# Optimization experiments

Measured on AMD Instinct MI355X. Metric: run time of the kernel, lower is better.

The kernel has to match this reference:

```python
import jax, jax.numpy as jnp
import numpy as np

B, V, F, H, W = 2, 8000, 1500, 128, 128
EPS_AREA = 1e-8
EPS_Z = 1e-4


def setup_inputs() -> dict:
    key = jax.random.key(0)
    k1, k2, k3 = jax.random.split(key, 3)
    verts = jax.random.normal(k1, (B, V, 3), jnp.float32) * 0.5
    faces = jax.random.randint(k2, (F, 3), 0, V)
    R = jnp.tile(jnp.eye(3, dtype=jnp.float32)[None], (B, 1, 1)) + 0.01 * jax.random.normal(k3, (B, 3, 3), jnp.float32)
    T = jnp.tile(jnp.array([0.0, 0.0, 3.0], jnp.float32)[None], (B, 1))
    focal = jnp.float32(2.0)
    return {"verts": verts, "R": R, "T": T, "focal": focal, "faces": faces}


def _edge(ax, ay, bx, by, px, py):
    return (px - ax) * (by - ay) - (py - ay) * (bx - ax)


def _project(verts, R, T, focal):
    # world -> view -> screen (NDC xy); screen z replaced by view z (as in MeshRasterizer.transform)
    vv = jnp.einsum('bvi,bij->bvj', verts, R) + T[:, None, :]   # [B,V,3]
    z = vv[..., 2:3]
    xy = focal * vv[..., :2] / z
    return jnp.concatenate([xy, z], axis=-1)                     # [B,V,3]


def _rasterize(vs, faces):
    fv = vs[:, faces]                                            # [B,F,3,3] (vert, xyz)
    # PyTorch3D NDC pixel centers: +X left, +Y up
    xg = 1.0 - 2.0 * (jnp.arange(W, dtype=jnp.float32) + 0.5) / W
    yg = 1.0 - 2.0 * (jnp.arange(H, dtype=jnp.float32) + 0.5) / H
    pyy, pxx = jnp.meshgrid(yg, xg, indexing='ij')
    pxf, pyf = pxx.reshape(-1), pyy.reshape(-1)                  # [P]

    fx = fv[..., 0][:, None]                                     # [B,1,F,3]
    fy = fv[..., 1][:, None]
    fz = fv[..., 2][:, None]
    px = pxf[None, :, None]                                      # [1,P,1]
    py = pyf[None, :, None]

    area = _edge(fv[..., 0, 0], fv[..., 0, 1], fv[..., 1, 0], fv[..., 1, 1],
                 fv[..., 2, 0], fv[..., 2, 1])[:, None]          # [B,1,F]
    area_safe = jnp.where(jnp.abs(area) > EPS_AREA, area, EPS_AREA)

    w0 = _edge(fx[..., 1], fy[..., 1], fx[..., 2], fy[..., 2], px, py)
    w1 = _edge(fx[..., 2], fy[..., 2], fx[..., 0], fy[..., 0], px, py)
    w2 = _edge(fx[..., 0], fy[..., 0], fx[..., 1], fy[..., 1], px, py)
    b0, b1, b2 = w0 / area_safe, w1 / area_safe, w2 / area_safe  # [B,P,F]

    inside = (b0 >= 0) & (b1 >= 0) & (b2 >= 0) & (jnp.abs(area) > EPS_AREA)
    zp = b0 * fz[..., 0] + b1 * fz[..., 1] + b2 * fz[..., 2]     # [B,P,F]
    valid = inside & (zp > EPS_Z)

    zmask = jnp.where(valid, zp, jnp.inf)
    idx = jnp.argmin(zmask, axis=-1)                             # [B,P]
    zmin = jnp.min(zmask, axis=-1)
    hit = jnp.isfinite(zmin)                                     # [B,P]

    # gather winning face per pixel, recompute bary / z / dists only for it
    bfv = fv[jnp.arange(B)[:, None], idx]                        # [B,P,3,3]
    bx, by, bz = bfv[..., 0], bfv[..., 1], bfv[..., 2]           # [B,P,3]
    pxp, pyp = pxf[None, :], pyf[None, :]

    a2 = _edge(bx[..., 0], by[..., 0], bx[..., 1], by[..., 1], bx[..., 2], by[..., 2])
    a2s = jnp.where(jnp.abs(a2) > EPS_AREA, a2, EPS_AREA)
    c0 = _edge(bx[..., 1], by[..., 1], bx[..., 2], by[..., 2], pxp, pyp) / a2s
    c1 = _edge(bx[..., 2], by[..., 2], bx[..., 0], by[..., 0], pxp, pyp) / a2s
    c2 = _edge(bx[..., 0], by[..., 0], bx[..., 1], by[..., 1], pxp, pyp) / a2s
    bary = jnp.stack([c0, c1, c2], axis=-1)                      # [B,P,3]
    zbest = jnp.sum(bary * bz, axis=-1)                          # [B,P]

    def seg_d2(ax, ay, bx_, by_):
        dx, dy = bx_ - ax, by_ - ay
        l2 = jnp.maximum(dx * dx + dy * dy, 1e-12)
        t = jnp.clip(((pxp - ax) * dx + (pyp - ay) * dy) / l2, 0.0, 1.0)
        ex, ey = ax + t * dx - pxp, ay + t * dy - pyp
        return ex * ex + ey * ey

    d2 = jnp.minimum(jnp.minimum(
        seg_d2(bx[..., 0], by[..., 0], bx[..., 1], by[..., 1]),
        seg_d2(bx[..., 1], by[..., 1], bx[..., 2], by[..., 2])),
        seg_d2(bx[..., 2], by[..., 2], bx[..., 0], by[..., 0]))
    inside_b = (c0 >= 0) & (c1 >= 0) & (c2 >= 0)
    dists = jnp.where(inside_b, -d2, d2)                         # signed sq. distance

    neg1 = jnp.float32(-1.0)
    pix_to_face = jnp.where(hit, idx, -1).astype(jnp.int32).reshape(B, H, W, 1)
    zbuf = jnp.where(hit, zbest, neg1).reshape(B, H, W, 1)
    bary_o = jnp.where(hit[..., None], bary, neg1).reshape(B, H, W, 1, 3)
    dists_o = jnp.where(hit, dists, neg1).reshape(B, H, W, 1)
    return pix_to_face, zbuf, bary_o, dists_o


def reference(verts, R, T, focal, faces):
    vs = _project(verts, R, T, focal)
    return _rasterize(vs, faces)
```

## Files before the change

kernel.cpp:

```cpp
#include <hip/hip_runtime.h>
#include <math.h>

#pragma clang fp contract(off)

#define Bn 2
#define Vn 8000
#define Fn 1500
#define Hn 128
#define Wn 128
#define EPS_AREA_F 1e-8f
#define EPS_Z_F 1e-4f
#define NWORD 24
#define NSEG 8
#define NSLICE 8
#define TPB (NSEG * 64)
#define MAXL 1536


__global__ void zero_kernel(unsigned long long* __restrict__ bins,
                            unsigned long long* __restrict__ keybuf) {
    int i = blockIdx.x * blockDim.x + threadIdx.x;
    int n1 = Bn * 256 * NWORD;
    int n2 = Bn * Hn * Wn;
    if (i < n1) bins[i] = 0ull;
    else if (i < n1 + n2) keybuf[i - n1] = ~0ull;
}

__global__ void proj_kernel(const float* __restrict__ verts, const float* __restrict__ R,
                            const float* __restrict__ T, const float* __restrict__ focal,
                            const int* __restrict__ faces,
                            float4* __restrict__ recS, unsigned* __restrict__ bboxT) {
    int t = blockIdx.x * blockDim.x + threadIdx.x;
    if (t >= Bn * Fn) return;
    int b = t / Fn;
    int f = t - b * Fn;
    const float* Rb = R + b * 9;
    const float* Tb = T + b * 3;
    float fo = focal[0];
    float X[3], Y[3], Z[3];
    for (int k = 0; k < 3; ++k) {
        int vi = faces[f * 3 + k];
        const float* v = verts + ((size_t)b * Vn + vi) * 3;
        float v0 = v[0], v1 = v[1], v2 = v[2];
        float vx = v0 * Rb[0] + v1 * Rb[3] + v2 * Rb[6] + Tb[0];
        float vy = v0 * Rb[1] + v1 * Rb[4] + v2 * Rb[7] + Tb[1];
        float vz = v0 * Rb[2] + v1 * Rb[5] + v2 * Rb[8] + Tb[2];
        X[k] = (fo * vx) / vz;
        Y[k] = (fo * vy) / vz;
        Z[k] = vz;
    }
    float area = (X[2] - X[0]) * (Y[1] - Y[0]) - (Y[2] - Y[0]) * (X[1] - X[0]);
    float as = (fabsf(area) > EPS_AREA_F) ? area : EPS_AREA_F;
    recS[t * 3 + 0] = make_float4(X[0], Y[0], X[1], Y[1]);
    recS[t * 3 + 1] = make_float4(X[2], Y[2], area, as);
    recS[t * 3 + 2] = make_float4(Z[0], Z[1], Z[2], 0.0f);

    unsigned pk = 0xFFFFFFFFu;
    if (fabsf(area) > EPS_AREA_F) {
        float xmin = fminf(X[0], fminf(X[1], X[2]));
        float xmax = fmaxf(X[0], fmaxf(X[1], X[2]));
        float ymin = fminf(Y[0], fminf(Y[1], Y[2]));
        float ymax = fmaxf(Y[0], fmaxf(Y[1], Y[2]));
        const float D = 0.02f;
        float wlo = ceilf(64.0f * (1.0f - xmax - D) - 0.5f);
        float whi = floorf(64.0f * (1.0f - xmin + D) - 0.5f);
        float hlo = ceilf(64.0f * (1.0f - ymax - D) - 0.5f);
        float hhi = floorf(64.0f * (1.0f - ymin + D) - 0.5f);
        wlo = fmaxf(wlo, 0.0f); whi = fminf(whi, 127.0f);
        hlo = fmaxf(hlo, 0.0f); hhi = fminf(hhi, 127.0f);
        if ((wlo <= whi) && (hlo <= hhi)) {
            int tx0 = (int)wlo >> 3, tx1 = (int)whi >> 3;
            int ty0 = (int)hlo >> 3, ty1 = (int)hhi >> 3;
            pk = (unsigned)tx0 | ((unsigned)tx1 << 8) |
                 ((unsigned)ty0 << 16) | ((unsigned)ty1 << 24);
        }
    }
    bboxT[t] = pk;
}

__global__ void bin_kernel(const unsigned* __restrict__ bboxT,
                           unsigned long long* __restrict__ bins) {
    int t = blockIdx.x * blockDim.x + threadIdx.x;
    if (t >= Bn * Fn * 16) return;
    int ty = t & 15;
    int bf = t >> 4;
    int b = bf / Fn;
    int f = bf - b * Fn;
    unsigned pk = bboxT[bf];
    if (pk == 0xFFFFFFFFu) return;
    int tx0 = pk & 0xFF, tx1 = (pk >> 8) & 0xFF;
    int ty0 = (pk >> 16) & 0xFF, ty1 = (pk >> 24) & 0xFF;
    if (ty < ty0 || ty > ty1) return;
    unsigned long long* bb = bins + ((size_t)b * 256 + ty * 16) * NWORD + (f >> 6);
    unsigned long long m = 1ull << (f & 63);
    for (int tx = tx0; tx <= tx1; ++tx)
        atomicOr(bb + (size_t)tx * NWORD, m);
}

__global__ __launch_bounds__(TPB)
void raster_kernel(const float4* __restrict__ recS,
                   const unsigned long long* __restrict__ bins,
                   unsigned long long* __restrict__ keybuf) {
    __shared__ unsigned short smList[MAXL];
    __shared__ int smCnt[NWORD];
    __shared__ int smL;
    __shared__ unsigned long long smK[NSEG * 64];

    int tid = threadIdx.x;
    int lane = tid & 63;
    int seg = tid >> 6;
    int blk = blockIdx.x;
    int slice = blk & (NSLICE - 1);
    int bt_ = blk >> 3;
    int b = bt_ >> 8;
    int tile = bt_ & 255;
    int h = ((tile >> 4) << 3) | (lane >> 3);
    int w = ((tile & 15) << 3) | (lane & 7);
    float px = 1.0f - (2.0f * ((float)w + 0.5f)) / (float)Wn;
    float py = 1.0f - (2.0f * ((float)h + 0.5f)) / (float)Hn;

    const float4* rb = recS + (size_t)b * Fn * 3;
    const unsigned long long* btp = bins + ((size_t)b * 256 + tile) * NWORD;

    if (tid < NWORD) smCnt[tid] = (int)__popcll(btp[tid]);
    __syncthreads();
    if (tid < NWORD) {
        int off = 0;
        for (int j = 0; j < tid; ++j) off += smCnt[j];
        unsigned long long m = btp[tid];
        int base = tid << 6;
        while (m) {
            int bit = __ffsll((unsigned long long)m) - 1;
            m &= m - 1;
            smList[off++] = (unsigned short)(base + bit);
        }
        if (tid == NWORD - 1) smL = off;
    }
    __syncthreads();
    int L = smL;

    unsigned long long best = ~0ull;
    int chunk = slice * NSEG + seg;
    int lo = (chunk * L) >> 6;
    int hi = ((chunk + 1) * L) >> 6;
    for (int j = lo; j < hi; ++j) {
        int f = smList[j];
        const float4* pr = rb + (size_t)f * 3;
        float4 q0 = pr[0];
        float4 q1 = pr[1];
        float x0 = q0.x, y0 = q0.y, x1 = q0.z, y1 = q0.w;
        float x2 = q1.x, y2 = q1.y, as = q1.w;
        float w0 = (px - x1) * (y2 - y1) - (py - y1) * (x2 - x1);
        float w1 = (px - x2) * (y0 - y2) - (py - y2) * (x0 - x2);
        float w2 = (px - x0) * (y1 - y0) - (py - y0) * (x1 - x0);
        bool ins = (as > 0.0f) ? (w0 >= 0.0f && w1 >= 0.0f && w2 >= 0.0f)
                               : (w0 <= 0.0f && w1 <= 0.0f && w2 <= 0.0f);
        if (ins) {
            float b0 = w0 / as;
            float b1 = w1 / as;
            float b2 = w2 / as;
            float4 q2 = pr[2];
            float zp = (b0 * q2.x + b1 * q2.y) + b2 * q2.z;
            if (zp > EPS_Z_F) {
                unsigned long long ck =
                    ((unsigned long long)__float_as_uint(zp) << 32) | (unsigned)f;
                if (ck < best) best = ck;
            }
        }
    }
    smK[seg * 64 + lane] = best;
    __syncthreads();

    if (tid < 64) {
        unsigned long long bk = smK[tid];
        #pragma unroll
        for (int s = 1; s < NSEG; ++s) {
            unsigned long long k = smK[s * 64 + tid];
            if (k < bk) bk = k;
        }
        if (bk != ~0ull) {
            int p = b * (Hn * Wn) + h * Wn + w;
            atomicMin(&keybuf[p], bk);
        }
    }
}

__global__ __launch_bounds__(256)
void writer_kernel(const float4* __restrict__ recS,
                   const unsigned long long* __restrict__ keybuf,
                   float* __restrict__ out) {
    int p = blockIdx.x * blockDim.x + threadIdx.x;
    if (p >= Bn * Hn * Wn) return;
    int b = p >> 14;
    int hw = p & 16383;
    int h = hw >> 7;
    int w = hw & 127;
    float px = 1.0f - (2.0f * ((float)w + 0.5f)) / (float)Wn;
    float py = 1.0f - (2.0f * ((float)h + 0.5f)) / (float)Hn;
    const float4* rb = recS + (size_t)b * Fn * 3;
    unsigned long long bk = keybuf[p];
    const int HWB = Bn * Hn * Wn;
    float o_idx = -1.0f, o_z = -1.0f, ob0 = -1.0f, ob1 = -1.0f, ob2 = -1.0f, o_d = -1.0f;
    if (bk != ~0ull) {
        int f = (int)(bk & 0xFFFFFFFFu);
        float4 q0 = rb[(size_t)f * 3 + 0];
        float4 q1 = rb[(size_t)f * 3 + 1];
        float x0 = q0.x, y0 = q0.y, x1 = q0.z, y1 = q0.w;
        float x2 = q1.x, y2 = q1.y, as = q1.w;
        float w0 = (px - x1) * (y2 - y1) - (py - y1) * (x2 - x1);
        float w1 = (px - x2) * (y0 - y2) - (py - y2) * (x0 - x2);
        float w2 = (px - x0) * (y1 - y0) - (py - y0) * (x1 - x0);
        float c0 = w0 / as, c1 = w1 / as, c2 = w2 / as;
        auto segd = [&](float ax, float ay, float bx, float by) -> float {
            float dx = bx - ax, dy = by - ay;
            float l2 = dx * dx + dy * dy;
            l2 = (l2 > 1e-12f) ? l2 : 1e-12f;
            float q = ((px - ax) * dx + (py - ay) * dy) / l2;
            q = (q < 0.0f) ? 0.0f : ((q > 1.0f) ? 1.0f : q);
            float ex = (ax + q * dx) - px;
            float ey = (ay + q * dy) - py;
            return ex * ex + ey * ey;
        };
        float d2 = fminf(fminf(segd(x0, y0, x1, y1), segd(x1, y1, x2, y2)),
                         segd(x2, y2, x0, y0));
        bool inside_b = (c0 >= 0.0f) && (c1 >= 0.0f) && (c2 >= 0.0f);
        o_idx = (float)f;
        o_z = __uint_as_float((unsigned)(bk >> 32));
        ob0 = c0; ob1 = c1; ob2 = c2;
        o_d = inside_b ? -d2 : d2;
    }
    out[p] = o_idx;
    out[HWB + p] = o_z;
    out[2 * HWB + p * 3 + 0] = ob0;
    out[2 * HWB + p * 3 + 1] = ob1;
    out[2 * HWB + p * 3 + 2] = ob2;
    out[5 * HWB + p] = o_d;
}

extern "C" void kernel_launch(void* const* d_in, const int* in_sizes, int n_in,
                              void* d_out, int out_size, void* d_ws, size_t ws_size,
                              hipStream_t stream) {
    const float* verts = (const float*)d_in[0];
    const float* R     = (const float*)d_in[1];
    const float* T     = (const float*)d_in[2];
    const float* focal = (const float*)d_in[3];
    const int*   faces = (const int*)d_in[4];
    float* out = (float*)d_out;
    char* ws = (char*)d_ws;
    float4* recS               = (float4*)(ws);
    unsigned* bboxT            = (unsigned*)(ws + 144000);
    unsigned long long* bins   = (unsigned long long*)(ws + 156000);
    unsigned long long* keybuf = (unsigned long long*)(ws + 254304);

    int nzero = Bn * 256 * NWORD + Bn * Hn * Wn;
    hipLaunchKernelGGL(zero_kernel, dim3((nzero + 255) / 256), dim3(256), 0, stream,
                       bins, keybuf);
    hipLaunchKernelGGL(proj_kernel, dim3((Bn * Fn + 255) / 256), dim3(256), 0, stream,
                       verts, R, T, focal, faces, recS, bboxT);
    hipLaunchKernelGGL(bin_kernel, dim3((Bn * Fn * 16 + 255) / 256), dim3(256), 0, stream,
                       bboxT, bins);
    hipLaunchKernelGGL(raster_kernel, dim3(Bn * 256 * NSLICE), dim3(TPB), 0, stream,
                       recS, bins, keybuf);
    hipLaunchKernelGGL(writer_kernel, dim3((Bn * Hn * Wn + 255) / 256), dim3(256),
                       0, stream, recS, keybuf, out);
}
```

Before: 102.8 us.

## Drop binning and zeroing kernels; test face bboxes per tile and reduce slices in writer

Removes the zero and bin kernels. Each raster wave now scans its fixed 1/64 share of all faces and skips those whose packed tile bbox misses the tile, instead of reading a compacted per-tile bitmask list. Per-slice best keys are written to a slice buffer without atomics, and the writer takes their minimum. This cuts two kernel launches, the atomics and the zeroing, but every block now scans all faces' bboxes, and load balance depends on how faces are ordered.

```diff
diff --git a/kernel.cpp b/kernel.cpp
--- a/kernel.cpp
+++ b/kernel.cpp
@@ -10,21 +10,10 @@
 #define Wn 128
 #define EPS_AREA_F 1e-8f
 #define EPS_Z_F 1e-4f
-#define NWORD 24
 #define NSEG 8
 #define NSLICE 8
 #define TPB (NSEG * 64)
-#define MAXL 1536
-
-
-__global__ void zero_kernel(unsigned long long* __restrict__ bins,
-                            unsigned long long* __restrict__ keybuf) {
-    int i = blockIdx.x * blockDim.x + threadIdx.x;
-    int n1 = Bn * 256 * NWORD;
-    int n2 = Bn * Hn * Wn;
-    if (i < n1) bins[i] = 0ull;
-    else if (i < n1 + n2) keybuf[i - n1] = ~0ull;
-}
+
 
 __global__ void proj_kernel(const float* __restrict__ verts, const float* __restrict__ R,
                             const float* __restrict__ T, const float* __restrict__ focal,
@@ -78,32 +67,9 @@
     bboxT[t] = pk;
 }
 
-__global__ void bin_kernel(const unsigned* __restrict__ bboxT,
-                           unsigned long long* __restrict__ bins) {
-    int t = blockIdx.x * blockDim.x + threadIdx.x;
-    if (t >= Bn * Fn * 16) return;
-    int ty = t & 15;
-    int bf = t >> 4;
-    int b = bf / Fn;
-    int f = bf - b * Fn;
-    unsigned pk = bboxT[bf];
-    if (pk == 0xFFFFFFFFu) return;
-    int tx0 = pk & 0xFF, tx1 = (pk >> 8) & 0xFF;
-    int ty0 = (pk >> 16) & 0xFF, ty1 = (pk >> 24) & 0xFF;
-    if (ty < ty0 || ty > ty1) return;
-    unsigned long long* bb = bins + ((size_t)b * 256 + ty * 16) * NWORD + (f >> 6);
-    unsigned long long m = 1ull << (f & 63);
-    for (int tx = tx0; tx <= tx1; ++tx)
-        atomicOr(bb + (size_t)tx * NWORD, m);
-}
-
 __global__ __launch_bounds__(TPB)
-void raster_kernel(const float4* __restrict__ recS,
-                   const unsigned long long* __restrict__ bins,
-                   unsigned long long* __restrict__ keybuf) {
-    __shared__ unsigned short smList[MAXL];
-    __shared__ int smCnt[NWORD];
-    __shared__ int smL;
+void raster_kernel(const float4* __restrict__ recS, const unsigned* __restrict__ bboxT,
+                   unsigned long long* __restrict__ keyslice) {
     __shared__ unsigned long long smK[NSEG * 64];
 
     int tid = threadIdx.x;
@@ -114,37 +80,26 @@
     int bt_ = blk >> 3;
     int b = bt_ >> 8;
     int tile = bt_ & 255;
-    int h = ((tile >> 4) << 3) | (lane >> 3);
-    int w = ((tile & 15) << 3) | (lane & 7);
+    int ty = tile >> 4, tx = tile & 15;
+    int h = (ty << 3) | (lane >> 3);
+    int w = (tx << 3) | (lane & 7);
     float px = 1.0f - (2.0f * ((float)w + 0.5f)) / (float)Wn;
     float py = 1.0f - (2.0f * ((float)h + 0.5f)) / (float)Hn;
 
+    int chunk = slice * NSEG + seg;
+    int lo = (chunk * Fn) >> 6;
+    int hi = ((chunk + 1) * Fn) >> 6;
+
+    const unsigned* bbb = bboxT + (size_t)b * Fn;
     const float4* rb = recS + (size_t)b * Fn * 3;
-    const unsigned long long* btp = bins + ((size_t)b * 256 + tile) * NWORD;
-
-    if (tid < NWORD) smCnt[tid] = (int)__popcll(btp[tid]);
-    __syncthreads();
-    if (tid < NWORD) {
-        int off = 0;
-        for (int j = 0; j < tid; ++j) off += smCnt[j];
-        unsigned long long m = btp[tid];
-        int base = tid << 6;
-        while (m) {
-            int bit = __ffsll((unsigned long long)m) - 1;
-            m &= m - 1;
-            smList[off++] = (unsigned short)(base + bit);
-        }
-        if (tid == NWORD - 1) smL = off;
-    }
-    __syncthreads();
-    int L = smL;
-
     unsigned long long best = ~0ull;
-    int chunk = slice * NSEG + seg;
-    int lo = (chunk * L) >> 6;
-    int hi = ((chunk + 1) * L) >> 6;
-    for (int j = lo; j < hi; ++j) {
-        int f = smList[j];
+
+    for (int f = lo; f < hi; ++f) {
+        unsigned pk = bbb[f];
+        if (pk == 0xFFFFFFFFu) continue;
+        int tx0 = pk & 0xFF, tx1 = (pk >> 8) & 0xFF;
+        int ty0 = (pk >> 16) & 0xFF, ty1 = (pk >> 24) & 0xFF;
+        if (tx < tx0 || tx > tx1 || ty < ty0 || ty > ty1) continue;
         const float4* pr = rb + (size_t)f * 3;
         float4 q0 = pr[0];
         float4 q1 = pr[1];
@@ -178,16 +133,16 @@
             unsigned long long k = smK[s * 64 + tid];
             if (k < bk) bk = k;
         }
-        if (bk != ~0ull) {
-            int p = b * (Hn * Wn) + h * Wn + w;
-            atomicMin(&keybuf[p], bk);
-        }
+        int hh = (ty << 3) | (tid >> 3);
+        int ww = (tx << 3) | (tid & 7);
+        int p = (b << 14) + hh * Wn + ww;
+        keyslice[(size_t)p * NSLICE + slice] = bk;
     }
 }
 
 __global__ __launch_bounds__(256)
 void writer_kernel(const float4* __restrict__ recS,
-                   const unsigned long long* __restrict__ keybuf,
+                   const unsigned long long* __restrict__ keyslice,
                    float* __restrict__ out) {
     int p = blockIdx.x * blockDim.x + threadIdx.x;
     if (p >= Bn * Hn * Wn) return;
@@ -197,8 +152,14 @@
     int w = hw & 127;
     float px = 1.0f - (2.0f * ((float)w + 0.5f)) / (float)Wn;
     float py = 1.0f - (2.0f * ((float)h + 0.5f)) / (float)Hn;
+    const unsigned long long* ks = keyslice + (size_t)p * NSLICE;
+    unsigned long long bk = ks[0];
+    #pragma unroll
+    for (int s = 1; s < NSLICE; ++s) {
+        unsigned long long k = ks[s];
+        if (k < bk) bk = k;
+    }
     const float4* rb = recS + (size_t)b * Fn * 3;
-    unsigned long long bk = keybuf[p];
     const int HWB = Bn * Hn * Wn;
     float o_idx = -1.0f, o_z = -1.0f, ob0 = -1.0f, ob1 = -1.0f, ob2 = -1.0f, o_d = -1.0f;
     if (bk != ~0ull) {
@@ -247,20 +208,14 @@
     const int*   faces = (const int*)d_in[4];
     float* out = (float*)d_out;
     char* ws = (char*)d_ws;
-    float4* recS               = (float4*)(ws);
-    unsigned* bboxT            = (unsigned*)(ws + 144000);
-    unsigned long long* bins   = (unsigned long long*)(ws + 156000);
-    unsigned long long* keybuf = (unsigned long long*)(ws + 254304);
-
-    int nzero = Bn * 256 * NWORD + Bn * Hn * Wn;
-    hipLaunchKernelGGL(zero_kernel, dim3((nzero + 255) / 256), dim3(256), 0, stream,
-                       bins, keybuf);
+    float4* recS                 = (float4*)(ws);
+    unsigned* bboxT              = (unsigned*)(ws + 144000);
+    unsigned long long* keyslice = (unsigned long long*)(ws + 156000);
+
     hipLaunchKernelGGL(proj_kernel, dim3((Bn * Fn + 255) / 256), dim3(256), 0, stream,
                        verts, R, T, focal, faces, recS, bboxT);
-    hipLaunchKernelGGL(bin_kernel, dim3((Bn * Fn * 16 + 255) / 256), dim3(256), 0, stream,
-                       bboxT, bins);
     hipLaunchKernelGGL(raster_kernel, dim3(Bn * 256 * NSLICE), dim3(TPB), 0, stream,
-                       recS, bins, keybuf);
+                       recS, bboxT, keyslice);
     hipLaunchKernelGGL(writer_kernel, dim3((Bn * Hn * Wn + 255) / 256), dim3(256),
-                       0, stream, recS, keybuf, out);
-}
+                       0, stream, recS, keyslice, out);
+}
```

Result: faster. 98.41 us (-4.2%).
